# Kernel tuning notes

Measured on AMD Instinct MI355X. Metric: run time of the kernel, lower is better.

## Reference

```python
import jax, jax.numpy as jnp
import numpy as np

THRESH = 0.5
LENS = 0.5
DECAY = 0.5
IN_SIZE = 8
T = 784 // IN_SIZE  # 98 timesteps
H = 1024
OUT = 10
SKIP = (2, 3, 4)
N_BATCH = 1024


@jax.custom_vjp
def act_fun(x):
    return (x > THRESH).astype(x.dtype)

def _af_fwd(x):
    return act_fun(x), x

def _af_bwd(x, g):
    return (g * (jnp.abs(x - THRESH) < LENS).astype(g.dtype),)

act_fun.defvjp(_af_fwd, _af_bwd)


def _make_mask(dim, cycle):
    base = np.array([1 if t % cycle == 0 else 0 for t in range(T)], dtype=np.int32)
    return np.stack([np.roll(base, n) for n in range(dim)])  # [dim, T]


def setup_inputs() -> dict:
    key = jax.random.key(0)
    ks = jax.random.split(key, 9)
    inp = {
        "input": jax.random.uniform(ks[0], (N_BATCH, 784), dtype=jnp.float32),
        "W1": jax.random.normal(ks[1], (H, IN_SIZE), dtype=jnp.float32) * 0.1,
        "b1": jax.random.normal(ks[2], (H,), dtype=jnp.float32) * 0.01,
        "W2": jax.random.normal(ks[3], (H, H), dtype=jnp.float32) * 0.03,
        "b2": jax.random.normal(ks[4], (H,), dtype=jnp.float32) * 0.01,
        "W3": jax.random.normal(ks[5], (H, H), dtype=jnp.float32) * 0.03,
        "b3": jax.random.normal(ks[6], (H,), dtype=jnp.float32) * 0.01,
        "W4": jax.random.normal(ks[7], (OUT, H), dtype=jnp.float32) * 0.03,
        "b4": jax.random.normal(ks[8], (OUT,), dtype=jnp.float32) * 0.01,
        "mask1": jnp.asarray(_make_mask(H, SKIP[0])),
        "mask2": jnp.asarray(_make_mask(H, SKIP[1])),
        "mask3": jnp.asarray(_make_mask(H, SKIP[2])),
    }
    return inp


def _gather_steps(x):
    # Faithful replication of the original (buggy) slicing: start = step*IN_SIZE,
    # but if start >= T - IN_SIZE the model uses the LAST IN_SIZE pixels.
    starts = np.array([s * IN_SIZE if s * IN_SIZE < T - IN_SIZE else 784 - IN_SIZE
                       for s in range(T)])
    idx = starts[:, None] + np.arange(IN_SIZE)  # [T, IN_SIZE]
    return jnp.transpose(x[:, idx], (1, 0, 2))  # [T, N, IN_SIZE]


def reference(input, W1, b1, W2, b2, W3, b3, W4, b4, mask1, mask2, mask3):
    N = input.shape[0]
    xs = _gather_steps(input)            # [T, N, IN_SIZE]
    mk1 = mask1.T                         # [T, H]
    mk2 = mask2.T
    mk3 = mask3.T

    def upd(drive, mem, spike, mk):
        mkf = mk.astype(mem.dtype)
        new_mem = mem * DECAY * (1.0 - spike) + drive
        mem = jnp.where(mk == 0, mem, new_mem)
        spike = act_fun(mem) * mkf
        return mem, spike

    zeros = lambda d: jnp.zeros((N, d), dtype=input.dtype)
    carry0 = (zeros(H), zeros(H), zeros(H), zeros(H), zeros(H), zeros(H),
              jnp.zeros((N, OUT), dtype=input.dtype), zeros(H), zeros(H), zeros(H))

    def step(carry, inp):
        m1, s1, m2, s2, m3, s3, osum, ss1, ss2, ss3 = carry
        x, k1, k2, k3 = inp
        m1, s1 = upd(x @ W1.T + b1, m1, s1, k1)
        m2, s2 = upd(s1 @ W2.T + b2, m2, s2, k2)
        m3, s3 = upd(s2 @ W3.T + b3, m3, s3, k3)
        out = s3 @ W4.T + b4
        return (m1, s1, m2, s2, m3, s3, osum + out,
                ss1 + s1, ss2 + s2, ss3 + s3), None

    carry, _ = jax.lax.scan(step, carry0, (xs, mk1, mk2, mk3))
    _, _, _, _, _, _, osum, ss1, ss2, ss3 = carry

    tw = jnp.asarray(T, dtype=input.dtype)
    outputs = osum / tw
    denom = jnp.asarray(N * H * T, dtype=input.dtype)
    layer_fr = jnp.stack([ss1.sum() / denom, ss2.sum() / denom, ss3.sum() / denom])
    hidden_spk = (ss1 / tw, ss2 / tw, ss3 / tw)
    return outputs, hidden_spk, layer_fr
```

## Files before the change

kernel.cpp:

```cpp
#include <hip/hip_runtime.h>

#define TTL 98
#define OUTD 10

typedef float f16v __attribute__((ext_vector_type(16)));
typedef short short8 __attribute__((ext_vector_type(8)));
typedef unsigned long ul2 __attribute__((ext_vector_type(2)));
typedef unsigned short ushort;

constexpr size_t MM = 1048576;
constexpr size_t OFF_OSUM = 5 * MM;
constexpr size_t OFF_XT   = OFF_OSUM + 10240;
constexpr size_t OFF_S1B  = OFF_XT + 802816;
constexpr size_t OFF_S2B  = OFF_S1B + 1605632;
constexpr size_t OFF_S1BT = OFF_S2B + 1103872;
constexpr size_t OFF_S2BT = OFF_S1BT + 1605632;
constexpr size_t OFF_W2S  = OFF_S2BT + 1103872;
constexpr size_t OFF_W3S  = OFF_W2S + 1572864;
constexpr size_t FIX_END  = OFF_W3S + 1585152;

constexpr size_t TAB_IDX2 = 0;
constexpr size_t TAB_IDX3 = 37632;
constexpr size_t TAB_CQ3  = 269696;
constexpr size_t TAB_L2   = 304192;
constexpr size_t TAB_L3   = 337984;

__device__ inline void split3(float w, ushort& h, ushort& m, ushort& l) {
    unsigned u = __float_as_uint(w);
    h = (ushort)(u >> 16);
    float r1 = w - __uint_as_float(u & 0xFFFF0000u);
    unsigned u1 = __float_as_uint(r1);
    m = (ushort)(u1 >> 16);
    float r2 = r1 - __uint_as_float(u1 & 0xFFFF0000u);
    l = (ushort)(__float_as_uint(r2) >> 16);
}

__device__ inline short8 expand8(unsigned x) {
    union { unsigned u[4]; short8 v; } r;
#pragma unroll
    for (int q = 0; q < 4; ++q) {
        unsigned b = x >> (2 * q);
        r.u[q] = ((b & 1u) * 0x3F80u) | ((b & 2u) ? 0x3F800000u : 0u);
    }
    return r.v;
}

__device__ inline short8 ldsAF(const ushort* base) {
    union { unsigned long u[2]; short8 s; } r;
    r.u[0] = *(const unsigned long*)(base);
    r.u[1] = *(const unsigned long*)(base + 4);
    return r.s;
}
__device__ inline void ldsWR(ushort* dst, ul2 v) {
    *(unsigned long*)(dst) = v[0];
    *(unsigned long*)(dst + 4) = v[1];
}

__global__ __launch_bounds__(256) void kSplit(
    const float* __restrict__ W2, const float* __restrict__ W3,
    ushort* __restrict__ W2S, ushort* __restrict__ W3S)
{
    int id = blockIdx.x * 256 + threadIdx.x;
    if (id < 1048576) {
        int p = id >> 19, rem = id & 524287, i = rem >> 9, q = rem & 511;
        ushort h, m, l;
        split3(W2[i * 1024 + 2 * q + p], h, m, l);
        size_t base = (size_t)p * 524288 + (size_t)i * 512 + q;
        W2S[base] = h; W2S[base + 1048576] = m; W2S[base + 2097152] = l;
    } else {
        int id2 = id - 1048576;
        if (id2 >= 1056768) return;
        int c = id2 / 352256, rem = id2 % 352256, i = rem / 344, q = rem % 344;
        int j = c + 3 * q;
        float w = (j < 1024) ? W3[i * 1024 + j] : 0.f;
        ushort h, m, l;
        split3(w, h, m, l);
        W3S[id2] = h; W3S[id2 + 1056768] = m; W3S[id2 + 2113536] = l;
    }
}

__global__ __launch_bounds__(256) void kPrep(const float* __restrict__ input,
                                             float* __restrict__ xT)
{
    __shared__ float Ls[64][65];
    int bx = blockIdx.x, tid = threadIdx.x;
    int wt = bx >> 4, nt = bx & 15;
    int w0 = wt * 64, n0 = nt * 64;
#pragma unroll
    for (int j = 0; j < 16; ++j) {
        int flat = tid + 256 * j;
        int a = flat >> 6, c = flat & 63;
        Ls[a][c] = (w0 + c < 784) ? input[(size_t)(n0 + a) * 784 + w0 + c] : 0.f;
    }
    __syncthreads();
#pragma unroll
    for (int j = 0; j < 16; ++j) {
        int flat = tid + 256 * j;
        int ii = flat >> 6, nn = flat & 63;
        if (w0 + ii < 784) xT[(size_t)(w0 + ii) * 1024 + n0 + nn] = Ls[nn][ii];
    }
}

__global__ __launch_bounds__(256) void kL1(
    const float* __restrict__ xT, const float* __restrict__ W1,
    const float* __restrict__ b1,
    unsigned long long* __restrict__ s1bits, float* __restrict__ ss1)
{
    int tid = threadIdx.x;
    int waveId = (blockIdx.x << 2) + (tid >> 6);
    int lane = tid & 63;
    int rowg = waveId >> 4;
    int nblk = waveId & 15;
    int i0 = rowg << 2;
    int n = (nblk << 6) + lane;
    float w[4][8], bb[4], mem[4], cnt[4];
#pragma unroll
    for (int r = 0; r < 4; ++r) {
#pragma unroll
        for (int e = 0; e < 8; ++e) w[r][e] = W1[(i0 + r) * 8 + e];
        bb[r] = b1[i0 + r]; mem[r] = 0.f; cnt[r] = 0.f;
    }
    float x[8], xn[8];
#pragma unroll
    for (int e = 0; e < 8; ++e) x[e] = xT[(size_t)e * 1024 + n];
    for (int t = 0; t < 12; ++t) {
        int st1 = ((t + 1) * 8 < TTL - 8) ? (t + 1) * 8 : (784 - 8);
#pragma unroll
        for (int e = 0; e < 8; ++e) xn[e] = xT[(size_t)(st1 + e) * 1024 + n];
#pragma unroll
        for (int r = 0; r < 4; ++r) {
            if (((t ^ (i0 + r)) & 1) == 0) {
                float d = bb[r];
#pragma unroll
                for (int e = 0; e < 8; ++e) d += w[r][e] * x[e];
                float m = mem[r] * 0.5f + d;
                mem[r] = m;
                bool sp = m > 0.5f;
                unsigned long long bm = __ballot(sp);
                if (lane == 0) s1bits[(size_t)(t * 512 + ((i0 + r) >> 1)) * 16 + nblk] = bm;
                if (sp) cnt[r] += 1.f;
            }
        }
#pragma unroll
        for (int e = 0; e < 8; ++e) x[e] = xn[e];
    }
    float dd[4];
#pragma unroll
    for (int r = 0; r < 4; ++r) {
        float d = bb[r];
#pragma unroll
        for (int e = 0; e < 8; ++e) d += w[r][e] * x[e];
        dd[r] = d;
    }
#pragma unroll 1
    for (int t = 12; t < TTL; t += 2) {
#pragma unroll
        for (int h = 0; h < 2; ++h) {
#pragma unroll
            for (int rr = 0; rr < 2; ++rr) {
                int r = h + rr * 2;
                float m = mem[r] * 0.5f + dd[r];
                mem[r] = m;
                bool sp = m > 0.5f;
                unsigned long long bm = __ballot(sp);
                if (lane == 0) s1bits[(size_t)((t + h) * 512 + ((i0 + r) >> 1)) * 16 + nblk] = bm;
                if (sp) cnt[r] += 1.f;
            }
        }
    }
#pragma unroll
    for (int r = 0; r < 4; ++r) ss1[(size_t)(i0 + r) * 1024 + n] = cnt[r];
}

__global__ __launch_bounds__(256) void kTab2(
    int* __restrict__ idx2, int* __restrict__ idx3, int* __restrict__ cq3)
{
    __shared__ int f2[256], f3[256];
    __shared__ int sidx2[384], sidx3[320];
    int t = blockIdx.x, tid = threadIdx.x;
    int a2[4], a3[4];
    int l2 = 0, l3 = 0;
#pragma unroll
    for (int e = 0; e < 4; ++e) {
        int i = tid * 4 + e;
        int u = (t - i) % TTL; if (u < 0) u += TTL;
        a2[e] = (u % 3 == 0); a3[e] = (u % 4 == 0);
        l2 += a2[e]; l3 += a3[e];
    }
    f2[tid] = l2; f3[tid] = l3;
    __syncthreads();
    for (int s = 1; s < 256; s <<= 1) {
        int v2 = (tid >= s) ? f2[tid - s] : 0;
        int v3 = (tid >= s) ? f3[tid - s] : 0;
        __syncthreads();
        f2[tid] += v2; f3[tid] += v3;
        __syncthreads();
    }
    int o2 = f2[tid] - l2, o3 = f3[tid] - l3;
    int c2 = f2[255], c3 = f3[255];
#pragma unroll
    for (int e = 0; e < 4; ++e) {
        int i = tid * 4 + e;
        if (a2[e]) { sidx2[o2] = i; ++o2; }
        if (a3[e]) { sidx3[o3] = i; ++o3; }
    }
    __syncthreads();
    for (int k = tid; k < 384; k += 256) idx2[t * 384 + k] = (k < c2) ? sidx2[k] : -1;
    for (int k = tid; k < 320; k += 256) idx3[t * 320 + k] = (k < c3) ? sidx3[k] : -1;
    for (int k = tid; k < 352; k += 256) {
        int j = (k < c2) ? sidx2[k] : 0;
        cq3[t * 352 + k] = (j % 3) * 352256 + j / 3;
    }
}

template<int C, int NACT>
__global__ __launch_bounds__(256) void kListCF(int* __restrict__ list)
{
    int flat = blockIdx.x * 256 + threadIdx.x;
    if (flat >= 1024 * NACT) return;
    int i = flat / NACT, s = flat % NACT;
    int ri = i % 98;
    int k0 = (98 - ri + C - 1) / C;
    int kw = NACT - k0; if (kw < 0) kw = 0;
    int t = (s < kw) ? (ri + (k0 + s) * C - 98) : (ri + (s - kw) * C);
    int rk = 0;
    int r = t;
#pragma unroll
    for (int k = 0; k < NACT; ++k) {
        rk += (r < i) ? (i - r + 97) / 98 : 0;
        r -= C; if (r < 0) r += 98;
    }
    list[i * NACT + s] = (t << 10) | rk;
}

template<int K>
__global__ __launch_bounds__(256) void kXb(const unsigned* __restrict__ in,
                                           unsigned* __restrict__ out, int t0)
{
    constexpr int Kw = K / 32;
    __shared__ unsigned L[1024];
    int bx = blockIdx.x, tid = threadIdx.x;
    int tt = t0 + bx / Kw, kw = bx % Kw;
    const unsigned* ip = in + ((size_t)tt * K + kw * 32) * 32;
#pragma unroll
    for (int g = 0; g < 4; ++g) L[g * 256 + tid] = ip[g * 256 + tid];
    __syncthreads();
    unsigned* op = out + ((size_t)tt * Kw + kw) * 1024;
#pragma unroll
    for (int g = 0; g < 4; ++g) {
        int n = g * 256 + tid;
        int w = n >> 5, b = n & 31;
        unsigned acc = 0;
#pragma unroll
        for (int k = 0; k < 32; ++k) acc |= ((L[k * 32 + w] >> b) & 1u) << k;
        op[n] = acc;
    }
}

__global__ __launch_bounds__(256) void kXbG3A(
    const unsigned* __restrict__ s2b, unsigned* __restrict__ s2bT,
    const ushort* __restrict__ Ws, const int* __restrict__ idx3,
    const int* __restrict__ cq3, ushort* __restrict__ AW3, int t0)
{
    __shared__ unsigned L[1024];
    int bx = blockIdx.x, tid = threadIdx.x;
    int tloc = bx / 66, r66 = bx % 66;
    int t = t0 + tloc;
    if (r66 < 11) {
        int kw = r66;
        const unsigned* ip = s2b + ((size_t)t * 352 + kw * 32) * 32;
#pragma unroll
        for (int g = 0; g < 4; ++g) L[g * 256 + tid] = ip[g * 256 + tid];
        __syncthreads();
        unsigned* op = s2bT + ((size_t)t * 11 + kw) * 1024;
#pragma unroll
        for (int g = 0; g < 4; ++g) {
            int n = g * 256 + tid;
            int w = n >> 5, b = n & 31;
            unsigned acc = 0;
#pragma unroll
            for (int k = 0; k < 32; ++k) acc |= ((L[k * 32 + w] >> b) & 1u) << k;
            op[n] = acc;
        }
    } else {
        int blk = r66 - 11;
        int flat = blk * 256 + tid;
        int r = flat / 44, kg = flat % 44;
        int k0 = kg * 8;
        int v = idx3[t * 320 + r];
        int i = v < 0 ? 0 : v;
        const int* cq = cq3 + t * 352 + k0;
        int c0 = cq[0], c1 = cq[1], c2 = cq[2], c3 = cq[3],
            c4 = cq[4], c5 = cq[5], c6 = cq[6], c7 = cq[7];
        size_t ia = (size_t)i * 344;
#pragma unroll
        for (int pi = 0; pi < 3; ++pi) {
            const ushort* wp = Ws + (size_t)pi * 1056768 + ia;
            union { ushort us[8]; ul2 v2; } o;
            o.us[0] = wp[c0]; o.us[1] = wp[c1]; o.us[2] = wp[c2]; o.us[3] = wp[c3];
            o.us[4] = wp[c4]; o.us[5] = wp[c5]; o.us[6] = wp[c6]; o.us[7] = wp[c7];
            *(ul2*)(AW3 + ((size_t)tloc * 3 + pi) * 112640 + (size_t)r * 352 + k0) = o.v2;
        }
    }
}


__global__ __launch_bounds__(256) void kGM2K(
    const ushort* __restrict__ Ws, const unsigned* __restrict__ s1bT,
    const int* __restrict__ idx2, float* __restrict__ drive, int t0)
{
    __shared__ ushort As[2][3][64][36];
    int tid = threadIdx.x, bx = blockIdx.x;
    int tloc = bx / 24, rem = bx % 24;
    int mt = rem >> 2, nt4 = rem & 3;
    int t = t0 + tloc;
    int p = t & 1;
    int r0 = mt * 64, n0 = nt4 * 256;
    int ar = tid >> 2, ak8 = (tid & 3) * 8;
    int vR = idx2[t * 384 + r0 + ar];
    const ushort* Wrow = Ws + (size_t)p * 524288 + (size_t)(vR < 0 ? 0 : vR) * 512 + ak8;
    int wv = tid >> 6, lane = tid & 63;
    int mrow = lane & 31, kh8 = (lane >> 5) * 8;
    int nb = n0 + wv * 64 + mrow;
    f16v acc[2][2];
#pragma unroll
    for (int a = 0; a < 2; ++a)
#pragma unroll
        for (int b = 0; b < 2; ++b) acc[a][b] = (f16v)(0.f);

    ul2 c0r[3];
#pragma unroll
    for (int pi = 0; pi < 3; ++pi) c0r[pi] = *(const ul2*)(Wrow + (size_t)pi * 1048576);
#pragma unroll
    for (int pi = 0; pi < 3; ++pi) ldsWR(&As[0][pi][ar][ak8], c0r[pi]);
    ul2 nxt[3];
#pragma unroll
    for (int pi = 0; pi < 3; ++pi) nxt[pi] = *(const ul2*)(Wrow + (size_t)pi * 1048576 + 32);
    unsigned w4c[2];
#pragma unroll
    for (int jj = 0; jj < 2; ++jj) w4c[jj] = s1bT[(size_t)t * 16 * 1024 + nb + jj * 32];
    __syncthreads();

    int cur = 0;
    for (int kc = 0; kc < 512; kc += 32) {
        if (kc + 32 < 512) {
#pragma unroll
            for (int pi = 0; pi < 3; ++pi) ldsWR(&As[cur ^ 1][pi][ar][ak8], nxt[pi]);
        }
        unsigned w4n[2];
        if (kc + 32 < 512) {
#pragma unroll
            for (int jj = 0; jj < 2; ++jj)
                w4n[jj] = s1bT[((size_t)t * 16 + ((kc + 32) >> 5)) * 1024 + nb + jj * 32];
        }
        ul2 n2[3];
        if (kc + 64 < 512) {
#pragma unroll
            for (int pi = 0; pi < 3; ++pi)
                n2[pi] = *(const ul2*)(Wrow + (size_t)pi * 1048576 + kc + 64);
        }
#pragma unroll
        for (int s2 = 0; s2 < 2; ++s2) {
            int kcol = s2 * 16 + kh8;
            short8 bf[2];
#pragma unroll
            for (int jj = 0; jj < 2; ++jj) bf[jj] = expand8((w4c[jj] >> kcol) & 0xFFu);
#pragma unroll
            for (int wr2 = 0; wr2 < 2; ++wr2) {
                short8 af0 = ldsAF(&As[cur][0][wr2 * 32 + mrow][kcol]);
                short8 af1 = ldsAF(&As[cur][1][wr2 * 32 + mrow][kcol]);
                short8 af2 = ldsAF(&As[cur][2][wr2 * 32 + mrow][kcol]);
#pragma unroll
                for (int jj = 0; jj < 2; ++jj) {
                    acc[wr2][jj] = __builtin_amdgcn_mfma_f32_32x32x16_bf16(af2, bf[jj], acc[wr2][jj], 0, 0, 0);
                    acc[wr2][jj] = __builtin_amdgcn_mfma_f32_32x32x16_bf16(af1, bf[jj], acc[wr2][jj], 0, 0, 0);
                    acc[wr2][jj] = __builtin_amdgcn_mfma_f32_32x32x16_bf16(af0, bf[jj], acc[wr2][jj], 0, 0, 0);
                }
            }
        }
        __syncthreads();
        cur ^= 1;
        nxt[0] = n2[0]; nxt[1] = n2[1]; nxt[2] = n2[2];
        w4c[0] = w4n[0]; w4c[1] = w4n[1];
    }
#pragma unroll
    for (int wr2 = 0; wr2 < 2; ++wr2)
#pragma unroll
        for (int jj = 0; jj < 2; ++jj)
#pragma unroll
            for (int reg = 0; reg < 16; ++reg) {
                int rowl = r0 + wr2 * 32 + (reg & 3) + 8 * (reg >> 2) + 4 * (lane >> 5);
                drive[((size_t)tloc * 384 + rowl) * 1024 + nb + jj * 32] = acc[wr2][jj][reg];
            }
}

__global__ __launch_bounds__(256) void kGM3K(
    const ushort* __restrict__ AW3, const unsigned* __restrict__ s2bT,
    float* __restrict__ drive, int t0)
{
    __shared__ ushort As[2][3][64][36];
    int tid = threadIdx.x, bx = blockIdx.x;
    int tloc = bx / 20, rem = bx % 20;
    int mt = rem >> 2, nt4 = rem & 3;
    int t = t0 + tloc;
    int r0 = mt * 64, n0 = nt4 * 256;
    int ar = tid >> 2, ak8 = (tid & 3) * 8;
    const ushort* Ab = AW3 + (size_t)tloc * 337920 + (size_t)(r0 + ar) * 352 + ak8;
    int wv = tid >> 6, lane = tid & 63;
    int mrow = lane & 31, kh8 = (lane >> 5) * 8;
    int nb = n0 + wv * 64 + mrow;
    f16v acc[2][2];
#pragma unroll
    for (int a = 0; a < 2; ++a)
#pragma unroll
        for (int b = 0; b < 2; ++b) acc[a][b] = (f16v)(0.f);

    ul2 c0r[3];
#pragma unroll
    for (int pi = 0; pi < 3; ++pi) c0r[pi] = *(const ul2*)(Ab + (size_t)pi * 112640);
#pragma unroll
    for (int pi = 0; pi < 3; ++pi) ldsWR(&As[0][pi][ar][ak8], c0r[pi]);
    ul2 nxt[3];
#pragma unroll
    for (int pi = 0; pi < 3; ++pi) nxt[pi] = *(const ul2*)(Ab + (size_t)pi * 112640 + 32);
    unsigned w4c[2];
#pragma unroll
    for (int jj = 0; jj < 2; ++jj) w4c[jj] = s2bT[(size_t)t * 11 * 1024 + nb + jj * 32];
    __syncthreads();

    int cur = 0;
    for (int kc = 0; kc < 352; kc += 32) {
        if (kc + 32 < 352) {
#pragma unroll
            for (int pi = 0; pi < 3; ++pi) ldsWR(&As[cur ^ 1][pi][ar][ak8], nxt[pi]);
        }
        unsigned w4n[2];
        if (kc + 32 < 352) {
#pragma unroll
            for (int jj = 0; jj < 2; ++jj)
                w4n[jj] = s2bT[((size_t)t * 11 + ((kc + 32) >> 5)) * 1024 + nb + jj * 32];
        }
        ul2 n2[3];
        if (kc + 64 < 352) {
#pragma unroll
            for (int pi = 0; pi < 3; ++pi)
                n2[pi] = *(const ul2*)(Ab + (size_t)pi * 112640 + kc + 64);
        }
#pragma unroll
        for (int s2 = 0; s2 < 2; ++s2) {
            int kcol = s2 * 16 + kh8;
            short8 bf[2];
#pragma unroll
            for (int jj = 0; jj < 2; ++jj) bf[jj] = expand8((w4c[jj] >> kcol) & 0xFFu);
#pragma unroll
            for (int wr2 = 0; wr2 < 2; ++wr2) {
                short8 af0 = ldsAF(&As[cur][0][wr2 * 32 + mrow][kcol]);
                short8 af1 = ldsAF(&As[cur][1][wr2 * 32 + mrow][kcol]);
                short8 af2 = ldsAF(&As[cur][2][wr2 * 32 + mrow][kcol]);
#pragma unroll
                for (int jj = 0; jj < 2; ++jj) {
                    acc[wr2][jj] = __builtin_amdgcn_mfma_f32_32x32x16_bf16(af2, bf[jj], acc[wr2][jj], 0, 0, 0);
                    acc[wr2][jj] = __builtin_amdgcn_mfma_f32_32x32x16_bf16(af1, bf[jj], acc[wr2][jj], 0, 0, 0);
                    acc[wr2][jj] = __builtin_amdgcn_mfma_f32_32x32x16_bf16(af0, bf[jj], acc[wr2][jj], 0, 0, 0);
                }
            }
        }
        __syncthreads();
        cur ^= 1;
        nxt[0] = n2[0]; nxt[1] = n2[1]; nxt[2] = n2[2];
        w4c[0] = w4n[0]; w4c[1] = w4n[1];
    }
#pragma unroll
    for (int wr2 = 0; wr2 < 2; ++wr2)
#pragma unroll
        for (int jj = 0; jj < 2; ++jj)
#pragma unroll
            for (int reg = 0; reg < 16; ++reg) {
                int rowl = r0 + wr2 * 32 + (reg & 3) + 8 * (reg >> 2) + 4 * (lane >> 5);
                drive[((size_t)tloc * 320 + rowl) * 1024 + nb + jj * 32] = acc[wr2][jj][reg];
            }
}

template<int MP, int KBP, bool BITS, int NACT>
__global__ __launch_bounds__(256) void kRK(
    const float* __restrict__ drive, const float* __restrict__ bias,
    const int* __restrict__ list,
    float* __restrict__ mG, float* __restrict__ ssG,
    unsigned long long* __restrict__ bitsOut, int t0, int nt)
{
    int tid = threadIdx.x;
    int row = blockIdx.x >> 2;
    int wv  = ((blockIdx.x & 3) << 2) + (tid >> 6);
    int lane = tid & 63;
    int n = (wv << 6) + lane;
    size_t idx = (size_t)row * 1024 + n;
    float mv = mG[idx];
    float cnt = 0.f;
    float bv = bias[row];
    const int* lp = list + row * NACT;
    int t1 = t0 + nt;
    int s0 = 0;
    while (s0 < NACT && (lp[s0] >> 10) < t0) ++s0;
    int s1 = s0;
    while (s1 < NACT && (lp[s1] >> 10) < t1) ++s1;
    if (s0 < s1) {
        int v0 = lp[s0];
        float d0 = drive[((size_t)((v0 >> 10) - t0) * MP + (v0 & 1023)) * 1024 + n];
        int v1 = 0; float d1 = 0.f;
        if (s0 + 1 < s1) {
            v1 = lp[s0 + 1];
            d1 = drive[((size_t)((v1 >> 10) - t0) * MP + (v1 & 1023)) * 1024 + n];
        }
        for (int s = s0; s < s1; ++s) {
            int vc = v0;
            float dcur = d0;
            v0 = v1; d0 = d1;
            if (s + 2 < s1) {
                v1 = lp[s + 2];
                d1 = drive[((size_t)((v1 >> 10) - t0) * MP + (v1 & 1023)) * 1024 + n];
            }
            float d = dcur + bv;
            float m = mv * 0.5f + d;
            mv = m;
            bool sp = m > 0.5f;
            if (BITS) {
                unsigned long long bm = __ballot(sp);
                if (lane == 0) bitsOut[((size_t)(vc >> 10) * KBP + (vc & 1023)) * 16 + wv] = bm;
            }
            cnt += sp ? 1.f : 0.f;
        }
    }
    mG[idx] = mv;
    ssG[idx] += cnt;
}

__global__ __launch_bounds__(256) void kTail(
    const float* __restrict__ ssBase, const float* __restrict__ W4,
    float* __restrict__ osum, float* __restrict__ out, float* __restrict__ fr)
{
    int bx = blockIdx.x, tid = threadIdx.x;
    if (bx < 768) {
        __shared__ float Ls[64][65];
        __shared__ float red[4];
        int l = bx >> 8;
        int tile = bx & 255;
        int i0 = (tile >> 4) * 64, n0 = (tile & 15) * 64;
        const float* ss = ssBase + (size_t)l * MM;
        float* o = out + 10240 + (size_t)l * MM;
        float sum = 0.f;
#pragma unroll
        for (int j = 0; j < 16; ++j) {
            int flat = tid + 256 * j;
            int a = flat >> 6, c = flat & 63;
            float v = ss[(size_t)(i0 + a) * 1024 + n0 + c];
            Ls[a][c] = v;
            sum += v;
        }
        __syncthreads();
        for (int off = 32; off > 0; off >>= 1) sum += __shfl_down(sum, off, 64);
        if ((tid & 63) == 0) red[tid >> 6] = sum;
        __syncthreads();
        if (tid == 0) {
            float s = red[0] + red[1] + red[2] + red[3];
            atomicAdd(&fr[l], s * (1.0f / (1024.0f * 1024.0f * 98.0f)));
        }
#pragma unroll
        for (int j = 0; j < 16; ++j) {
            int flat = tid + 256 * j;
            int nn = flat >> 6, ii = flat & 63;
            o[(size_t)(n0 + nn) * 1024 + i0 + ii] = Ls[ii][nn] * (1.0f / 98.0f);
        }
    } else {
        int b = bx - 768;
        int ks = b >> 4, nt = b & 15;
        int n = nt * 64 + (tid & 63);
        int og = tid >> 6;
        const float* ss3 = ssBase + (size_t)2 * MM;
        float a0 = 0.f, a1 = 0.f, a2 = 0.f;
        int k0 = ks * 256;
        for (int k = k0; k < k0 + 256; ++k) {
            float v = ss3[(size_t)k * 1024 + n];
            a0 += v * W4[og * 1024 + k];
            a1 += v * W4[(og + 4) * 1024 + k];
            if (og < 2) a2 += v * W4[(og + 8) * 1024 + k];
        }
        atomicAdd(&osum[n * OUTD + og], a0);
        atomicAdd(&osum[n * OUTD + og + 4], a1);
        if (og < 2) atomicAdd(&osum[n * OUTD + og + 8], a2);
    }
}

__global__ void kOut(const float* __restrict__ osum, const float* __restrict__ b4,
                     float* __restrict__ out)
{
    int idx = blockIdx.x * 256 + threadIdx.x;
    if (idx < 1024 * OUTD) out[idx] = osum[idx] * (1.0f / 98.0f) + b4[idx % OUTD];
}

extern "C" void kernel_launch(void* const* d_in, const int* in_sizes, int n_in,
                              void* d_out, int out_size, void* d_ws, size_t ws_size,
                              hipStream_t stream)
{
    const float* input = (const float*)d_in[0];
    const float* W1    = (const float*)d_in[1];
    const float* b1    = (const float*)d_in[2];
    const float* W2    = (const float*)d_in[3];
    const float* b2    = (const float*)d_in[4];
    const float* W3    = (const float*)d_in[5];
    const float* b3    = (const float*)d_in[6];
    const float* W4    = (const float*)d_in[7];
    const float* b4    = (const float*)d_in[8];

    float* ws = (float*)d_ws;
    float* ss1  = ws;
    float* ss2  = ws + MM;
    float* ss3  = ws + 2 * MM;
    float* m2   = ws + 3 * MM;
    float* m3   = ws + 4 * MM;
    float* osum = ws + OFF_OSUM;
    float* xT   = ws + OFF_XT;
    int*   tabs = (int*)(ws + OFF_XT);
    int* idx2  = tabs + TAB_IDX2;
    int* idx3  = tabs + TAB_IDX3;
    int* cq3   = tabs + TAB_CQ3;
    int* list2 = tabs + TAB_L2;
    int* list3 = tabs + TAB_L3;
    unsigned int* s1b  = (unsigned int*)(ws + OFF_S1B);
    unsigned int* s2b  = (unsigned int*)(ws + OFF_S2B);
    unsigned int* s1bT = (unsigned int*)(ws + OFF_S1BT);
    unsigned int* s2bT = (unsigned int*)(ws + OFF_S2BT);
    ushort* W2S = (ushort*)(ws + OFF_W2S);
    ushort* W3S = (ushort*)(ws + OFF_W3S);
    float* out  = (float*)d_out;

    size_t availF = ws_size / sizeof(float);
    constexpr size_t PER_T = 84480 + 384 * 1024 + 320 * 1024;
    int tc = 14;
    const int cands[7] = {98, 66, 49, 40, 33, 25, 14};
    for (int ci = 0; ci < 7; ++ci) {
        if (FIX_END + (size_t)cands[ci] * PER_T <= availF) { tc = cands[ci]; break; }
    }
    ushort* AW3 = (ushort*)(ws + FIX_END);
    float* drv2 = ws + FIX_END + (size_t)tc * 84480;
    float* drv3 = drv2 + (size_t)tc * 384 * 1024;

    hipMemsetAsync(ws, 0, (5 * MM + 10240) * sizeof(float), stream);
    hipMemsetAsync(s2b, 0, 1103872 * sizeof(unsigned int), stream);
    hipMemsetAsync(out + 3155968, 0, 3 * sizeof(float), stream);

    kSplit<<<8224, 256, 0, stream>>>(W2, W3, W2S, W3S);
    kPrep<<<208, 256, 0, stream>>>(input, xT);
    kL1<<<1024, 256, 0, stream>>>(xT, W1, b1, (unsigned long long*)s1b, ss1);
    kTab2<<<98, 256, 0, stream>>>(idx2, idx3, cq3);
    kListCF<3, 33><<<132, 256, 0, stream>>>(list2);
    kListCF<4, 25><<<100, 256, 0, stream>>>(list3);
    kXb<512><<<1568, 256, 0, stream>>>(s1b, s1bT, 0);

    for (int t0 = 0; t0 < TTL; t0 += tc) {
        int nt = (TTL - t0 < tc) ? (TTL - t0) : tc;
        kGM2K<<<nt * 24, 256, 0, stream>>>(W2S, s1bT, idx2, drv2, t0);
        kRK<384, 352, true, 33><<<4096, 256, 0, stream>>>(drv2, b2, list2, m2, ss2,
                                                          (unsigned long long*)s2b, t0, nt);
        kXbG3A<<<nt * 66, 256, 0, stream>>>(s2b, s2bT, W3S, idx3, cq3, AW3, t0);
        kGM3K<<<nt * 20, 256, 0, stream>>>(AW3, s2bT, drv3, t0);
        kRK<320, 0, false, 25><<<4096, 256, 0, stream>>>(drv3, b3, list3, m3, ss3,
                                                         nullptr, t0, nt);
    }

    kTail<<<832, 256, 0, stream>>>(ss1, W4, osum, out, out + 3155968);
    kOut<<<40, 256, 0, stream>>>(osum, b4, out);
}
```

Measured before the change: 519.7 us.

## Software-pipeline layer-2 and layer-3 chunks by fusing their GEMM and recurrence launches

The time-chunk loop is restructured so layer-2 work for chunk c+1 and layer-3 work for chunk c run in the same launches. Fused kernels kGMF and kRKF dispatch on block index to the corresponding GEMM or recurrence body, which fills the GPU better and removes launches. The AW3 per-timestep size is doubled and a smaller chunk candidate is added, which changes workspace sizing and may pick a smaller chunk count. Correctness depends on AW3, drv2 and drv3 not being overwritten while a fused launch still reads them.

```diff
diff --git a/kernel.cpp b/kernel.cpp
--- a/kernel.cpp
+++ b/kernel.cpp
@@ -25,6 +25,8 @@
 constexpr size_t TAB_L2   = 304192;
 constexpr size_t TAB_L3   = 337984;
 
+constexpr size_t AW3_PER_T = 168960;
+
 __device__ inline void split3(float w, ushort& h, ushort& m, ushort& l) {
     unsigned u = __float_as_uint(w);
     h = (ushort)(u >> 16);
@@ -55,6 +57,7 @@
     *(unsigned long*)(dst) = v[0];
     *(unsigned long*)(dst + 4) = v[1];
 }
+#define ASOFF(cur, pi, row, col) (((((cur)*3 + (pi))*64 + (row))*36) + (col))
 
 __global__ __launch_bounds__(256) void kSplit(
     const float* __restrict__ W2, const float* __restrict__ W3,
@@ -305,12 +308,11 @@
 }
 
 
-__global__ __launch_bounds__(256) void kGM2K(
+__device__ __forceinline__ void gm2_body(
+    int bx, int tid, ushort* AsR,
     const ushort* __restrict__ Ws, const unsigned* __restrict__ s1bT,
     const int* __restrict__ idx2, float* __restrict__ drive, int t0)
 {
-    __shared__ ushort As[2][3][64][36];
-    int tid = threadIdx.x, bx = blockIdx.x;
     int tloc = bx / 24, rem = bx % 24;
     int mt = rem >> 2, nt4 = rem & 3;
     int t = t0 + tloc;
@@ -332,7 +334,7 @@
 #pragma unroll
     for (int pi = 0; pi < 3; ++pi) c0r[pi] = *(const ul2*)(Wrow + (size_t)pi * 1048576);
 #pragma unroll
-    for (int pi = 0; pi < 3; ++pi) ldsWR(&As[0][pi][ar][ak8], c0r[pi]);
+    for (int pi = 0; pi < 3; ++pi) ldsWR(&AsR[ASOFF(0, pi, ar, ak8)], c0r[pi]);
     ul2 nxt[3];
 #pragma unroll
     for (int pi = 0; pi < 3; ++pi) nxt[pi] = *(const ul2*)(Wrow + (size_t)pi * 1048576 + 32);
@@ -345,7 +347,7 @@
     for (int kc = 0; kc < 512; kc += 32) {
         if (kc + 32 < 512) {
 #pragma unroll
-            for (int pi = 0; pi < 3; ++pi) ldsWR(&As[cur ^ 1][pi][ar][ak8], nxt[pi]);
+            for (int pi = 0; pi < 3; ++pi) ldsWR(&AsR[ASOFF(cur ^ 1, pi, ar, ak8)], nxt[pi]);
         }
         unsigned w4n[2];
         if (kc + 32 < 512) {
@@ -367,9 +369,9 @@
             for (int jj = 0; jj < 2; ++jj) bf[jj] = expand8((w4c[jj] >> kcol) & 0xFFu);
 #pragma unroll
             for (int wr2 = 0; wr2 < 2; ++wr2) {
-                short8 af0 = ldsAF(&As[cur][0][wr2 * 32 + mrow][kcol]);
-                short8 af1 = ldsAF(&As[cur][1][wr2 * 32 + mrow][kcol]);
-                short8 af2 = ldsAF(&As[cur][2][wr2 * 32 + mrow][kcol]);
+                short8 af0 = ldsAF(&AsR[ASOFF(cur, 0, wr2 * 32 + mrow, kcol)]);
+                short8 af1 = ldsAF(&AsR[ASOFF(cur, 1, wr2 * 32 + mrow, kcol)]);
+                short8 af2 = ldsAF(&AsR[ASOFF(cur, 2, wr2 * 32 + mrow, kcol)]);
 #pragma unroll
                 for (int jj = 0; jj < 2; ++jj) {
                     acc[wr2][jj] = __builtin_amdgcn_mfma_f32_32x32x16_bf16(af2, bf[jj], acc[wr2][jj], 0, 0, 0);
@@ -394,12 +396,11 @@
             }
 }
 
-__global__ __launch_bounds__(256) void kGM3K(
+__device__ __forceinline__ void gm3_body(
+    int bx, int tid, ushort* AsR,
     const ushort* __restrict__ AW3, const unsigned* __restrict__ s2bT,
     float* __restrict__ drive, int t0)
 {
-    __shared__ ushort As[2][3][64][36];
-    int tid = threadIdx.x, bx = blockIdx.x;
     int tloc = bx / 20, rem = bx % 20;
     int mt = rem >> 2, nt4 = rem & 3;
     int t = t0 + tloc;
@@ -419,7 +420,7 @@
 #pragma unroll
     for (int pi = 0; pi < 3; ++pi) c0r[pi] = *(const ul2*)(Ab + (size_t)pi * 112640);
 #pragma unroll
-    for (int pi = 0; pi < 3; ++pi) ldsWR(&As[0][pi][ar][ak8], c0r[pi]);
+    for (int pi = 0; pi < 3; ++pi) ldsWR(&AsR[ASOFF(0, pi, ar, ak8)], c0r[pi]);
     ul2 nxt[3];
 #pragma unroll
     for (int pi = 0; pi < 3; ++pi) nxt[pi] = *(const ul2*)(Ab + (size_t)pi * 112640 + 32);
@@ -432,7 +433,7 @@
     for (int kc = 0; kc < 352; kc += 32) {
         if (kc + 32 < 352) {
 #pragma unroll
-            for (int pi = 0; pi < 3; ++pi) ldsWR(&As[cur ^ 1][pi][ar][ak8], nxt[pi]);
+            for (int pi = 0; pi < 3; ++pi) ldsWR(&AsR[ASOFF(cur ^ 1, pi, ar, ak8)], nxt[pi]);
         }
         unsigned w4n[2];
         if (kc + 32 < 352) {
@@ -454,9 +455,9 @@
             for (int jj = 0; jj < 2; ++jj) bf[jj] = expand8((w4c[jj] >> kcol) & 0xFFu);
 #pragma unroll
             for (int wr2 = 0; wr2 < 2; ++wr2) {
-                short8 af0 = ldsAF(&As[cur][0][wr2 * 32 + mrow][kcol]);
-                short8 af1 = ldsAF(&As[cur][1][wr2 * 32 + mrow][kcol]);
-                short8 af2 = ldsAF(&As[cur][2][wr2 * 32 + mrow][kcol]);
+                short8 af0 = ldsAF(&AsR[ASOFF(cur, 0, wr2 * 32 + mrow, kcol)]);
+                short8 af1 = ldsAF(&AsR[ASOFF(cur, 1, wr2 * 32 + mrow, kcol)]);
+                short8 af2 = ldsAF(&AsR[ASOFF(cur, 2, wr2 * 32 + mrow, kcol)]);
 #pragma unroll
                 for (int jj = 0; jj < 2; ++jj) {
                     acc[wr2][jj] = __builtin_amdgcn_mfma_f32_32x32x16_bf16(af2, bf[jj], acc[wr2][jj], 0, 0, 0);
@@ -481,16 +482,43 @@
             }
 }
 
+__global__ __launch_bounds__(256) void kGM2K(
+    const ushort* __restrict__ Ws, const unsigned* __restrict__ s1bT,
+    const int* __restrict__ idx2, float* __restrict__ drive, int t0)
+{
+    __shared__ ushort AsR[2 * 3 * 64 * 36];
+    gm2_body(blockIdx.x, threadIdx.x, AsR, Ws, s1bT, idx2, drive, t0);
+}
+__global__ __launch_bounds__(256) void kGM3K(
+    const ushort* __restrict__ AW3, const unsigned* __restrict__ s2bT,
+    float* __restrict__ drive, int t0)
+{
+    __shared__ ushort AsR[2 * 3 * 64 * 36];
+    gm3_body(blockIdx.x, threadIdx.x, AsR, AW3, s2bT, drive, t0);
+}
+
+__global__ __launch_bounds__(256) void kGMF(
+    const ushort* __restrict__ W2S, const unsigned* __restrict__ s1bT,
+    const int* __restrict__ idx2, float* __restrict__ drv2, int t0_2, int n2blocks,
+    const ushort* __restrict__ AW3, const unsigned* __restrict__ s2bT,
+    float* __restrict__ drv3, int t0_3)
+{
+    __shared__ ushort AsR[2 * 3 * 64 * 36];
+    int bx = blockIdx.x;
+    if (bx < n2blocks) gm2_body(bx, threadIdx.x, AsR, W2S, s1bT, idx2, drv2, t0_2);
+    else               gm3_body(bx - n2blocks, threadIdx.x, AsR, AW3, s2bT, drv3, t0_3);
+}
+
 template<int MP, int KBP, bool BITS, int NACT>
-__global__ __launch_bounds__(256) void kRK(
+__device__ __forceinline__ void rk_body(
+    int bx, int tid,
     const float* __restrict__ drive, const float* __restrict__ bias,
     const int* __restrict__ list,
     float* __restrict__ mG, float* __restrict__ ssG,
     unsigned long long* __restrict__ bitsOut, int t0, int nt)
 {
-    int tid = threadIdx.x;
-    int row = blockIdx.x >> 2;
-    int wv  = ((blockIdx.x & 3) << 2) + (tid >> 6);
+    int row = bx >> 2;
+    int wv  = ((bx & 3) << 2) + (tid >> 6);
     int lane = tid & 63;
     int n = (wv << 6) + lane;
     size_t idx = (size_t)row * 1024 + n;
@@ -532,6 +560,34 @@
     }
     mG[idx] = mv;
     ssG[idx] += cnt;
+}
+
+template<int MP, int KBP, bool BITS, int NACT>
+__global__ __launch_bounds__(256) void kRK(
+    const float* __restrict__ drive, const float* __restrict__ bias,
+    const int* __restrict__ list,
+    float* __restrict__ mG, float* __restrict__ ssG,
+    unsigned long long* __restrict__ bitsOut, int t0, int nt)
+{
+    rk_body<MP, KBP, BITS, NACT>(blockIdx.x, threadIdx.x, drive, bias, list,
+                                 mG, ssG, bitsOut, t0, nt);
+}
+
+__global__ __launch_bounds__(256) void kRKF(
+    const float* __restrict__ drv3, const float* __restrict__ b3,
+    const int* __restrict__ list3, float* __restrict__ m3, float* __restrict__ ss3,
+    int t0_3, int nt3,
+    const float* __restrict__ drv2, const float* __restrict__ b2,
+    const int* __restrict__ list2, float* __restrict__ m2, float* __restrict__ ss2,
+    unsigned long long* __restrict__ s2bits, int t0_2, int nt2)
+{
+    int bx = blockIdx.x;
+    if (bx < 4096)
+        rk_body<320, 0, false, 25>(bx, threadIdx.x, drv3, b3, list3, m3, ss3,
+                                   nullptr, t0_3, nt3);
+    else
+        rk_body<384, 352, true, 33>(bx - 4096, threadIdx.x, drv2, b2, list2, m2, ss2,
+                                    s2bits, t0_2, nt2);
 }
 
 __global__ __launch_bounds__(256) void kTail(
@@ -634,14 +690,14 @@
     float* out  = (float*)d_out;
 
     size_t availF = ws_size / sizeof(float);
-    constexpr size_t PER_T = 84480 + 384 * 1024 + 320 * 1024;
-    int tc = 14;
-    const int cands[7] = {98, 66, 49, 40, 33, 25, 14};
-    for (int ci = 0; ci < 7; ++ci) {
+    constexpr size_t PER_T = AW3_PER_T + 384 * 1024 + 320 * 1024;
+    int tc = 10;
+    const int cands[8] = {98, 66, 49, 40, 33, 25, 14, 10};
+    for (int ci = 0; ci < 8; ++ci) {
         if (FIX_END + (size_t)cands[ci] * PER_T <= availF) { tc = cands[ci]; break; }
     }
     ushort* AW3 = (ushort*)(ws + FIX_END);
-    float* drv2 = ws + FIX_END + (size_t)tc * 84480;
+    float* drv2 = ws + FIX_END + (size_t)tc * AW3_PER_T;
     float* drv3 = drv2 + (size_t)tc * 384 * 1024;
 
     hipMemsetAsync(ws, 0, (5 * MM + 10240) * sizeof(float), stream);
@@ -656,16 +712,28 @@
     kListCF<4, 25><<<100, 256, 0, stream>>>(list3);
     kXb<512><<<1568, 256, 0, stream>>>(s1b, s1bT, 0);
 
-    for (int t0 = 0; t0 < TTL; t0 += tc) {
-        int nt = (TTL - t0 < tc) ? (TTL - t0) : tc;
-        kGM2K<<<nt * 24, 256, 0, stream>>>(W2S, s1bT, idx2, drv2, t0);
-        kRK<384, 352, true, 33><<<4096, 256, 0, stream>>>(drv2, b2, list2, m2, ss2,
-                                                          (unsigned long long*)s2b, t0, nt);
-        kXbG3A<<<nt * 66, 256, 0, stream>>>(s2b, s2bT, W3S, idx3, cq3, AW3, t0);
-        kGM3K<<<nt * 20, 256, 0, stream>>>(AW3, s2bT, drv3, t0);
-        kRK<320, 0, false, 25><<<4096, 256, 0, stream>>>(drv3, b3, list3, m3, ss3,
-                                                         nullptr, t0, nt);
-    }
+    int nc = (TTL + tc - 1) / tc;
+    auto ntOf = [&](int c) { int t0c = c * tc; return (TTL - t0c < tc) ? (TTL - t0c) : tc; };
+
+    kGM2K<<<ntOf(0) * 24, 256, 0, stream>>>(W2S, s1bT, idx2, drv2, 0);
+    kRK<384, 352, true, 33><<<4096, 256, 0, stream>>>(drv2, b2, list2, m2, ss2,
+                                                      (unsigned long long*)s2b, 0, ntOf(0));
+    kXbG3A<<<ntOf(0) * 66, 256, 0, stream>>>(s2b, s2bT, W3S, idx3, cq3, AW3, 0);
+
+    for (int c = 0; c + 1 < nc; ++c) {
+        int t03 = c * tc, t02 = (c + 1) * tc;
+        int n2b = ntOf(c + 1) * 24, n3b = ntOf(c) * 20;
+        kGMF<<<n2b + n3b, 256, 0, stream>>>(W2S, s1bT, idx2, drv2, t02, n2b,
+                                            AW3, s2bT, drv3, t03);
+        kRKF<<<8192, 256, 0, stream>>>(drv3, b3, list3, m3, ss3, t03, ntOf(c),
+                                       drv2, b2, list2, m2, ss2,
+                                       (unsigned long long*)s2b, t02, ntOf(c + 1));
+        kXbG3A<<<ntOf(c + 1) * 66, 256, 0, stream>>>(s2b, s2bT, W3S, idx3, cq3, AW3, t02);
+    }
+    int cl = nc - 1, t0l = cl * tc;
+    kGM3K<<<ntOf(cl) * 20, 256, 0, stream>>>(AW3, s2bT, drv3, t0l);
+    kRK<320, 0, false, 25><<<4096, 256, 0, stream>>>(drv3, b3, list3, m3, ss3,
+                                                     nullptr, t0l, ntOf(cl));
 
     kTail<<<832, 256, 0, stream>>>(ss1, W4, osum, out, out + 3155968);
     kOut<<<40, 256, 0, stream>>>(osum, b4, out);
```

Measured after the change: 518.7 us (median of 2 runs). No clear change (-0.2%).
